# Performance work log

Hardware: AMD Instinct MI355X
Metric: run time of the kernel (lower is better)

## Reference

```python
import jax, jax.numpy as jnp
import numpy as np
import math

N = 50000      # nodes per type
E = 800000     # edges per relation
IN = 256
OUT = 256
H = 8
DK = OUT // H  # 32
SQRT_DK = math.sqrt(DK)


def setup_inputs() -> dict:
    key = jax.random.key(0)
    ks = jax.random.split(key, 24)
    s = 0.02
    inp = {
        'h_A': jax.random.normal(ks[0], (N, IN), jnp.float32),
        'h_B': jax.random.normal(ks[1], (N, IN), jnp.float32),
        'src0': jax.random.randint(ks[2], (E,), 0, N, jnp.int32),
        'dst0': jax.random.randint(ks[3], (E,), 0, N, jnp.int32),
        'src1': jax.random.randint(ks[4], (E,), 0, N, jnp.int32),
        'dst1': jax.random.randint(ks[5], (E,), 0, N, jnp.int32),
        'src2': jax.random.randint(ks[6], (E,), 0, N, jnp.int32),
        'dst2': jax.random.randint(ks[7], (E,), 0, N, jnp.int32),
        # per-node-type linears (2 types): y = x @ W + b
        'Wk': jax.random.normal(ks[8], (2, IN, OUT), jnp.float32) * s,
        'bk': jnp.zeros((2, OUT), jnp.float32),
        'Wq': jax.random.normal(ks[9], (2, IN, OUT), jnp.float32) * s,
        'bq': jnp.zeros((2, OUT), jnp.float32),
        'Wv': jax.random.normal(ks[10], (2, IN, OUT), jnp.float32) * s,
        'bv': jnp.zeros((2, OUT), jnp.float32),
        'Wa': jax.random.normal(ks[11], (2, OUT, OUT), jnp.float32) * s,
        'ba': jnp.zeros((2, OUT), jnp.float32),
        # per-relation params (3 relations)
        'rel_att': jax.random.normal(ks[12], (3, H, DK, DK), jnp.float32) * (1.0 / math.sqrt(DK)),
        'rel_msg': jax.random.normal(ks[13], (3, H, DK, DK), jnp.float32) * (1.0 / math.sqrt(DK)),
        'rel_pri': jnp.ones((3, H), jnp.float32),
        'skip': jnp.ones((2,), jnp.float32),
    }
    return inp


def _relation_flow(k_src, v_src, q_dst, A_r, M_r, pri_r, src, dst):
    # k_src/v_src/q_dst: [N,H,DK] ; A_r,M_r: [H,DK,DK] ; pri_r: [H]
    k = jnp.einsum('bij,ijk->bik', k_src, A_r)
    v = jnp.einsum('bij,ijk->bik', v_src, M_r)
    # edge-wise dot: sum_d q[dst] * k[src] per head -> [E,H]
    score = jnp.einsum('ehd,ehd->eh', q_dst[dst], k[src]) * pri_r / SQRT_DK
    # edge softmax normalized by dst
    mx = jax.ops.segment_max(score, dst, num_segments=N)
    ex = jnp.exp(score - mx[dst])
    den = jax.ops.segment_sum(ex, dst, num_segments=N)
    attn = ex / den[dst]                       # [E,H]
    msg = v[src] * attn[:, :, None]            # [E,H,DK]
    return jax.ops.segment_sum(msg, dst, num_segments=N)  # [N,H,DK]


def reference(h_A, h_B, src0, dst0, src1, dst1, src2, dst2,
              Wk, bk, Wq, bq, Wv, bv, Wa, ba,
              rel_att, rel_msg, rel_pri, skip):
    h = [h_A, h_B]
    hd = lambda x: x.reshape(-1, H, DK)
    k = [hd(h[t] @ Wk[t] + bk[t]) for t in range(2)]
    q = [hd(h[t] @ Wq[t] + bq[t]) for t in range(2)]
    v = [hd(h[t] @ Wv[t] + bv[t]) for t in range(2)]

    # relations: r0: A->B, r1: B->A, r2: A->B
    t0 = _relation_flow(k[0], v[0], q[1], rel_att[0], rel_msg[0], rel_pri[0], src0, dst0)
    t1 = _relation_flow(k[1], v[1], q[0], rel_att[1], rel_msg[1], rel_pri[1], src1, dst1)
    t2 = _relation_flow(k[0], v[0], q[1], rel_att[2], rel_msg[2], rel_pri[2], src2, dst2)

    # cross_reducer='mean' over relations delivering to each dst type
    t_A = t1.reshape(N, OUT)
    t_B = ((t0 + t2) * 0.5).reshape(N, OUT)

    def out_for(tn, nid):
        alpha = jax.nn.sigmoid(skip[nid])
        trans = tn @ Wa[nid] + ba[nid]   # dropout is identity at eval
        return trans * alpha + h[nid] * (1.0 - alpha)

    new_h_A = out_for(t_A, 0)
    new_h_B = out_for(t_B, 1)
    return jnp.stack([new_h_A, new_h_B])  # [2, N, OUT]
```

## Files before the change

kernel.cpp:

```cpp
#include <hip/hip_runtime.h>
#include <math.h>

#define NN 50000
#define EE 800000
#define CC 256
#define NS (NN * CC)
#define NBK 782
#define BCAP 2048
#define P1T 2048
#define NT1 391
#define TOBF_BLKS 12500
#define PREP_BLKS 2568

typedef __attribute__((ext_vector_type(4))) float f32x4;
typedef __attribute__((ext_vector_type(8))) short bf16x8;
typedef __attribute__((ext_vector_type(4))) unsigned int u32x4;
typedef __attribute__((ext_vector_type(2))) unsigned int u32x2;

__device__ __forceinline__ float bf2f(unsigned int u) {
    union { unsigned int i; float f; } c; c.i = u << 16; return c.f;
}
__device__ __forceinline__ unsigned short f2bf(float f) {
    union { float f; unsigned int i; } c; c.f = f;
    unsigned int u = c.i;
    u += 0x7fffu + ((u >> 16) & 1u);
    return (unsigned short)(u >> 16);
}

#if __has_builtin(__builtin_amdgcn_cvt_f32_fp8) && __has_builtin(__builtin_amdgcn_cvt_pk_fp8_f32)
#define HW_FP8 1
#else
#define HW_FP8 0
#endif

__device__ __forceinline__ unsigned char sw_f2fp8(float f) {
    float a = fabsf(f);
    unsigned s = (f < 0.f) ? 0x80u : 0u;
    if (a >= 448.f) return (unsigned char)(s | 0x7Eu);
    if (a < 0.015625f) {
        int q = (int)(a * 512.f + 0.5f);
        return (unsigned char)(s | (unsigned)q);
    }
    int e = (int)floorf(log2f(a));
    float m = ldexpf(a, -e);
    int q = (int)(m * 8.f + 0.5f);
    if (q == 16) { q = 8; e += 1; }
    if (e > 8) return (unsigned char)(s | 0x7Eu);
    return (unsigned char)(s | ((unsigned)(e + 7) << 3) | (unsigned)(q - 8));
}
__device__ __forceinline__ float sw_fp82f(unsigned b) {
    unsigned s = (b & 0x80u) << 24;
    unsigned exp = (b >> 3) & 0xFu, man = b & 7u;
    float val = (exp == 0) ? ldexpf((float)man, -9)
                           : ldexpf((float)(8u | man), (int)exp - 10);
    unsigned r = __builtin_bit_cast(unsigned, val) | s;
    return __builtin_bit_cast(float, r);
}
__device__ __forceinline__ unsigned char f2fp8(float f) {
#if HW_FP8
    return (unsigned char)(__builtin_amdgcn_cvt_pk_fp8_f32(f, 0.f, 0, false) & 0xff);
#else
    return sw_f2fp8(f);
#endif
}
__device__ __forceinline__ float fp8sel(unsigned int w, int sel) {
#if HW_FP8
    switch (sel) {
        case 0: return __builtin_amdgcn_cvt_f32_fp8((int)w, 0);
        case 1: return __builtin_amdgcn_cvt_f32_fp8((int)w, 1);
        case 2: return __builtin_amdgcn_cvt_f32_fp8((int)w, 2);
        default: return __builtin_amdgcn_cvt_f32_fp8((int)w, 3);
    }
#else
    return sw_fp82f((w >> (sel * 8)) & 0xffu);
#endif
}

__global__ void setup_kernel(const float* __restrict__ hA, const float* __restrict__ hB,
                             unsigned short* __restrict__ h_bf,
                             const float* __restrict__ Wk, const float* __restrict__ bk,
                             const float* __restrict__ Wq, const float* __restrict__ bq,
                             const float* __restrict__ Wv, const float* __restrict__ bv,
                             const float* __restrict__ Wa,
                             const float* __restrict__ rel_att, const float* __restrict__ rel_msg,
                             unsigned short* __restrict__ WT, float* __restrict__ ball,
                             const int* __restrict__ d0, const int* __restrict__ d1,
                             const int* __restrict__ d2, int* __restrict__ bcnt)
{
    int b = blockIdx.x;
    const int ts[3] = {0, 1, 0};
    if (b < TOBF_BLKS) {
        int id = b * 256 + threadIdx.x;
        size_t base = (size_t)id * 8;
        const float* src = (base < (size_t)NS) ? (hA + base) : (hB + (base - NS));
        f32x4 a = *(const f32x4*)src;
        f32x4 bb2 = *(const f32x4*)(src + 4);
        u32x4 o;
        o[0] = (unsigned)f2bf(a[0]) | ((unsigned)f2bf(a[1]) << 16);
        o[1] = (unsigned)f2bf(a[2]) | ((unsigned)f2bf(a[3]) << 16);
        o[2] = (unsigned)f2bf(bb2[0]) | ((unsigned)f2bf(bb2[1]) << 16);
        o[3] = (unsigned)f2bf(bb2[2]) | ((unsigned)f2bf(bb2[3]) << 16);
        *(u32x4*)(h_bf + base) = o;
        return;
    }
    if (b >= TOBF_BLKS + PREP_BLKS) {
        int bb = b - (TOBF_BLKS + PREP_BLKS);
        int r = bb / NT1, tile = bb - r * NT1;
        const int* dp = r == 0 ? d0 : (r == 1 ? d1 : d2);
        __shared__ int hist[NBK];
        for (int i = threadIdx.x; i < NBK; i += 256) hist[i] = 0;
        __syncthreads();
        int base = tile * P1T;
        int lim = base + P1T; if (lim > EE) lim = EE;
        for (int i = base + threadIdx.x; i < lim; i += 256)
            atomicAdd(&hist[dp[i] >> 6], 1);
        __syncthreads();
        for (int i = threadIdx.x; i < NBK; i += 256)
            if (hist[i]) atomicAdd(&bcnt[r * NBK + i], hist[i]);
        return;
    }
    int id = (b - TOBF_BLKS) * 256 + threadIdx.x;
    if (id < 2 * 65536) {
        int t = id >> 16, rem = id & 65535;
        int n = rem >> 8, k = rem & 255;
        WT[t * 65536 + n * 256 + k] = f2bf(Wq[t * 65536 + k * 256 + n]);
    } else if (id < 5 * 65536) {
        int id2 = id - 2 * 65536;
        int r = id2 >> 16, rem = id2 & 65535;
        int n = rem >> 8, k = rem & 255;
        int h = n >> 5, j = n & 31;
        const float* wkb = Wk + ts[r] * 65536 + k * 256 + h * 32;
        const float* ab  = rel_att + r * 8192 + h * 1024 + j;
        float s = 0.f;
        #pragma unroll 8
        for (int d = 0; d < 32; ++d) s += wkb[d] * ab[d * 32];
        WT[(2 + r) * 65536 + n * 256 + k] = f2bf(s);
    } else if (id < 8 * 65536) {
        int id2 = id - 5 * 65536;
        int r = id2 >> 16, rem = id2 & 65535;
        int n = rem >> 8, k = rem & 255;
        int h = n >> 5, j = n & 31;
        const float* wvb = Wv + ts[r] * 65536 + k * 256 + h * 32;
        const float* mb  = rel_msg + r * 8192 + h * 1024 + j;
        float s = 0.f;
        #pragma unroll 8
        for (int d = 0; d < 32; ++d) s += wvb[d] * mb[d * 32];
        WT[(5 + r) * 65536 + n * 256 + k] = f2bf(s);
    } else if (id < 10 * 65536) {
        int id2 = id - 8 * 65536;
        int t = id2 >> 16, rem = id2 & 65535;
        int n = rem >> 8, k = rem & 255;
        WT[(8 + t) * 65536 + n * 256 + k] = f2bf(Wa[t * 65536 + k * 256 + n]);
    } else if (id < 10 * 65536 + 2048) {
        int id2 = id - 10 * 65536;
        int z = id2 >> 8, c = id2 & 255;
        float v;
        if (z < 2) {
            v = bq[z * 256 + c];
        } else if (z < 5) {
            int r = z - 2, h = c >> 5, j = c & 31;
            const float* bkb = bk + ts[r] * 256 + h * 32;
            const float* ab  = rel_att + r * 8192 + h * 1024 + j;
            v = 0.f;
            for (int d = 0; d < 32; ++d) v += bkb[d] * ab[d * 32];
        } else {
            int r = z - 5, h = c >> 5, j = c & 31;
            const float* bvb = bv + ts[r] * 256 + h * 32;
            const float* mb  = rel_msg + r * 8192 + h * 1024 + j;
            v = 0.f;
            for (int d = 0; d < 32; ++d) v += bvb[d] * mb[d * 32];
        }
        ball[z * 256 + c] = v;
    }
}

__global__ __launch_bounds__(1024) void bscan_kernel(const int* __restrict__ bcnt,
                                                     int* __restrict__ bbase,
                                                     int* __restrict__ bcur)
{
    int r = blockIdx.x;
    int t = threadIdx.x, lane = t & 63, w = t >> 6;
    __shared__ int wsum[16];
    int x = (t < NBK) ? bcnt[r * NBK + t] : 0;
    int v = x;
    #pragma unroll
    for (int ofs = 1; ofs < 64; ofs <<= 1) {
        int y = __shfl_up(v, ofs);
        if (lane >= ofs) v += y;
    }
    if (lane == 63) wsum[w] = v;
    __syncthreads();
    if (t < 16) {
        int wv = wsum[t];
        #pragma unroll
        for (int ofs = 1; ofs < 16; ofs <<= 1) {
            int y = __shfl_up(wv, ofs);
            if (t >= ofs) wv += y;
        }
        wsum[t] = wv;
    }
    __syncthreads();
    int excl = (w > 0 ? wsum[w - 1] : 0) + v - x;
    if (t < NBK) { bbase[r * (NBK + 1) + t] = excl; bcur[r * NBK + t] = excl; }
    if (t == NBK - 1) bbase[r * (NBK + 1) + NBK] = excl + x;
}

__global__ __launch_bounds__(256) void p1_kernel(const int* __restrict__ s0, const int* __restrict__ s1,
                                                 const int* __restrict__ s2,
                                                 const int* __restrict__ d0, const int* __restrict__ d1,
                                                 const int* __restrict__ d2,
                                                 int* __restrict__ bcur, unsigned int* __restrict__ srcS)
{
    int bb = blockIdx.x;
    int r = bb / NT1, tile = bb - r * NT1;
    const int* sp = r == 0 ? s0 : (r == 1 ? s1 : s2);
    const int* dp = r == 0 ? d0 : (r == 1 ? d1 : d2);
    __shared__ int hist[NBK];
    __shared__ int lbase[NBK];
    for (int i = threadIdx.x; i < NBK; i += 256) hist[i] = 0;
    __syncthreads();
    int base = tile * P1T;
    int lim = base + P1T; if (lim > EE) lim = EE;
    for (int i = base + threadIdx.x; i < lim; i += 256)
        atomicAdd(&hist[dp[i] >> 6], 1);
    __syncthreads();
    for (int i = threadIdx.x; i < NBK; i += 256)
        lbase[i] = hist[i] ? atomicAdd(&bcur[r * NBK + i], hist[i]) : 0;
    __syncthreads();
    unsigned int* out = srcS + (size_t)r * EE;
    for (int i = base + threadIdx.x; i < lim; i += 256) {
        int dv = dp[i];
        int bk = dv >> 6;
        int pos = atomicAdd(&lbase[bk], 1);
        out[pos] = ((unsigned)sp[i] << 6) | (unsigned)(dv & 63);
    }
}

__global__ __launch_bounds__(256) void p2_kernel(const int* __restrict__ bbase,
                                                 unsigned int* __restrict__ srcS,
                                                 int* __restrict__ offs)
{
    int r = blockIdx.x / NBK, bk = blockIdx.x - r * NBK;
    int base = bbase[r * (NBK + 1) + bk];
    int n = bbase[r * (NBK + 1) + bk + 1] - base;
    unsigned int* seg = srcS + (size_t)r * EE + base;
    __shared__ unsigned int vals[BCAP];
    __shared__ unsigned int sorted[BCAP];
    __shared__ int hist[64], hcur[64];
    int t = threadIdx.x;
    if (t < 64) hist[t] = 0;
    __syncthreads();
    for (int i = t; i < n; i += 256) {
        unsigned int v = seg[i];
        vals[i] = v;
        atomicAdd(&hist[v & 63], 1);
    }
    __syncthreads();
    if (t < 64) {
        int x = hist[t], v = x;
        #pragma unroll
        for (int ofs = 1; ofs < 64; ofs <<= 1) {
            int y = __shfl_up(v, ofs);
            if (t >= ofs) v += y;
        }
        int excl = v - x;
        hcur[t] = excl;
        int d = bk * 64 + t;
        if (d < NN) offs[r * (NN + 1) + d] = base + excl;
    }
    if (bk == NBK - 1 && t == 64) offs[r * (NN + 1) + NN] = EE;
    __syncthreads();
    for (int i = t; i < n; i += 256) {
        unsigned int v = vals[i];
        int pos = atomicAdd(&hcur[v & 63], 1);
        sorted[pos] = v >> 6;
    }
    __syncthreads();
    for (int i = t; i < n; i += 256) seg[i] = sorted[i];
}

__device__ __forceinline__ void gemm_body(const unsigned short* __restrict__ A,
                                          const unsigned short* __restrict__ W,
                                          const float* __restrict__ bias,
                                          unsigned short* __restrict__ Obf,
                                          unsigned char* __restrict__ Of8,
                                          int mBase, int nBase)
{
    __shared__ __align__(16) unsigned short As[128 * 64];
    __shared__ __align__(16) unsigned short Bs[128 * 64];

    int tid = threadIdx.x;
    int lane = tid & 63, wid = tid >> 6;
    int warpM = wid >> 1, warpN = wid & 1;

    f32x4 acc[4][4];
    #pragma unroll
    for (int i = 0; i < 4; ++i)
        #pragma unroll
        for (int j = 0; j < 4; ++j) acc[i][j] = (f32x4){0.f, 0.f, 0.f, 0.f};

    for (int kt = 0; kt < 4; ++kt) {
        int k0 = kt * 64;
        __syncthreads();
        #pragma unroll
        for (int i = 0; i < 4; ++i) {
            int c = tid + i * 256;
            int row = c >> 3, cc = c & 7;
            int gr = mBase + row; if (gr > NN - 1) gr = NN - 1;
            u32x4 av = *(const u32x4*)(A + (size_t)gr * CC + k0 + cc * 8);
            int sb = row * 128 + ((cc * 16) ^ ((row & 7) << 4));
            *(u32x4*)((char*)As + sb) = av;
            u32x4 bv = *(const u32x4*)(W + (nBase + row) * 256 + k0 + cc * 8);
            *(u32x4*)((char*)Bs + sb) = bv;
        }
        __syncthreads();
        #pragma unroll
        for (int kk = 0; kk < 2; ++kk) {
            bf16x8 af[4], bfr[4];
            int kb = kk * 64 + (lane >> 4) * 16;
            #pragma unroll
            for (int mi = 0; mi < 4; ++mi) {
                int row = warpM * 64 + mi * 16 + (lane & 15);
                int sb = row * 128 + (kb ^ ((row & 7) << 4));
                af[mi] = *(const bf16x8*)((const char*)As + sb);
            }
            #pragma unroll
            for (int ni = 0; ni < 4; ++ni) {
                int row = warpN * 64 + ni * 16 + (lane & 15);
                int sb = row * 128 + (kb ^ ((row & 7) << 4));
                bfr[ni] = *(const bf16x8*)((const char*)Bs + sb);
            }
            #pragma unroll
            for (int mi = 0; mi < 4; ++mi)
                #pragma unroll
                for (int ni = 0; ni < 4; ++ni)
                    acc[mi][ni] = __builtin_amdgcn_mfma_f32_16x16x32_bf16(af[mi], bfr[ni], acc[mi][ni], 0, 0, 0);
        }
    }

    #pragma unroll
    for (int mi = 0; mi < 4; ++mi) {
        #pragma unroll
        for (int ni = 0; ni < 4; ++ni) {
            int col = nBase + warpN * 64 + ni * 16 + (lane & 15);
            int row0 = mBase + warpM * 64 + mi * 16 + (lane >> 4) * 4;
            float b = bias[col];
            #pragma unroll
            for (int j = 0; j < 4; ++j) {
                int row = row0 + j;
                if (row < NN) {
                    float val = acc[mi][ni][j] + b;
                    if (Of8) Of8[(size_t)row * 512 + col] = f2fp8(val);
                    else     Obf[(size_t)row * 256 + col] = f2bf(val);
                }
            }
        }
    }
}

__global__ __launch_bounds__(256, 2)
void gemm8_kernel(const unsigned short* __restrict__ h_bf,
                  const unsigned short* __restrict__ WT, const float* __restrict__ ball,
                  unsigned short* __restrict__ Qb, unsigned char* __restrict__ KV0,
                  unsigned char* __restrict__ KV1, unsigned char* __restrict__ KV2)
{
    int bid = blockIdx.x;
    int mtile = bid >> 4;
    int rem = bid & 15;
    int z = rem >> 1;
    int ntile = rem & 1;
    const unsigned short* A = (z == 1 || z == 3 || z == 6) ? (h_bf + (size_t)NS) : h_bf;
    unsigned short* Obf = nullptr;
    unsigned char* Of8 = nullptr;
    switch (z) {
        case 0: Obf = Qb;               break;
        case 1: Obf = Qb + (size_t)NS;  break;
        case 2: Of8 = KV0;              break;
        case 3: Of8 = KV1;              break;
        case 4: Of8 = KV2;              break;
        case 5: Of8 = KV0 + 256;        break;
        case 6: Of8 = KV1 + 256;        break;
        default: Of8 = KV2 + 256;       break;
    }
    gemm_body(A, WT + z * 65536, ball + z * 256, Obf, Of8,
              mtile * 128, ntile * 128);
}

__global__ __launch_bounds__(256, 2)
void out_gemm_kernel(const unsigned short* __restrict__ A0, const unsigned short* __restrict__ A1,
                     const unsigned short* __restrict__ W0, const unsigned short* __restrict__ W1,
                     const float* __restrict__ b0, const float* __restrict__ b1,
                     float* __restrict__ OutF,
                     const float* __restrict__ hA, const float* __restrict__ hB,
                     const float* __restrict__ skip)
{
    int z = blockIdx.z;
    const unsigned short* A = z ? A1 : A0;
    const unsigned short* W = z ? W1 : W0;
    const float* bias = z ? b1 : b0;
    int mBase = blockIdx.x * 128;
    int nBase = blockIdx.y * 128;

    __shared__ __align__(16) unsigned short As[128 * 64];
    __shared__ __align__(16) unsigned short Bs[128 * 64];

    int tid = threadIdx.x;
    int lane = tid & 63, wid = tid >> 6;
    int warpM = wid >> 1, warpN = wid & 1;

    f32x4 acc[4][4];
    #pragma unroll
    for (int i = 0; i < 4; ++i)
        #pragma unroll
        for (int j = 0; j < 4; ++j) acc[i][j] = (f32x4){0.f, 0.f, 0.f, 0.f};

    for (int kt = 0; kt < 4; ++kt) {
        int k0 = kt * 64;
        __syncthreads();
        #pragma unroll
        for (int i = 0; i < 4; ++i) {
            int c = tid + i * 256;
            int row = c >> 3, cc = c & 7;
            int gr = mBase + row; if (gr > NN - 1) gr = NN - 1;
            u32x4 av = *(const u32x4*)(A + (size_t)gr * CC + k0 + cc * 8);
            int sb = row * 128 + ((cc * 16) ^ ((row & 7) << 4));
            *(u32x4*)((char*)As + sb) = av;
            u32x4 bv = *(const u32x4*)(W + (nBase + row) * 256 + k0 + cc * 8);
            *(u32x4*)((char*)Bs + sb) = bv;
        }
        __syncthreads();
        #pragma unroll
        for (int kk = 0; kk < 2; ++kk) {
            bf16x8 af[4], bfr[4];
            int kb = kk * 64 + (lane >> 4) * 16;
            #pragma unroll
            for (int mi = 0; mi < 4; ++mi) {
                int row = warpM * 64 + mi * 16 + (lane & 15);
                int sb = row * 128 + (kb ^ ((row & 7) << 4));
                af[mi] = *(const bf16x8*)((const char*)As + sb);
            }
            #pragma unroll
            for (int ni = 0; ni < 4; ++ni) {
                int row = warpN * 64 + ni * 16 + (lane & 15);
                int sb = row * 128 + (kb ^ ((row & 7) << 4));
                bfr[ni] = *(const bf16x8*)((const char*)Bs + sb);
            }
            #pragma unroll
            for (int mi = 0; mi < 4; ++mi)
                #pragma unroll
                for (int ni = 0; ni < 4; ++ni)
                    acc[mi][ni] = __builtin_amdgcn_mfma_f32_16x16x32_bf16(af[mi], bfr[ni], acc[mi][ni], 0, 0, 0);
        }
    }

    float alpha = 1.f / (1.f + __expf(-skip[z]));
    const float* hres = z ? hB : hA;

    #pragma unroll
    for (int mi = 0; mi < 4; ++mi) {
        #pragma unroll
        for (int ni = 0; ni < 4; ++ni) {
            int col = nBase + warpN * 64 + ni * 16 + (lane & 15);
            int row0 = mBase + warpM * 64 + mi * 16 + (lane >> 4) * 4;
            float b = bias[col];
            #pragma unroll
            for (int j = 0; j < 4; ++j) {
                int row = row0 + j;
                if (row < NN) {
                    float val = acc[mi][ni][j] + b;
                    float hv = hres[(size_t)row * CC + col];
                    OutF[(size_t)z * NS + (size_t)row * CC + col] = val * alpha + hv * (1.f - alpha);
                }
            }
        }
    }
}

__device__ __forceinline__ void agg_pass(const unsigned char* __restrict__ KV,
                                         const int* __restrict__ srcS,
                                         int beg, int end, int lane,
                                         float q0, float q1, float q2, float q3, float ps,
                                         float& o0, float& o1, float& o2, float& o3)
{
    float l = 0.f;
    float a0 = 0.f, a1 = 0.f, a2 = 0.f, a3 = 0.f;
    int n = end - beg;
    if (n > 0) {
        int p0 = beg + lane;
        int idx = srcS[p0 < end ? p0 : end - 1];
        int s = __shfl(idx, 0);
        unsigned int kw = *(const unsigned int*)(KV + (size_t)s * 512 + lane * 4);
        unsigned int vw = *(const unsigned int*)(KV + (size_t)s * 512 + 256 + lane * 4);
        for (int j = 0; j < n; ++j) {
            unsigned int kc = kw, vc = vw;
            int jn = j + 1;
            if (jn < n) {
                if ((jn & 63) == 0) {
                    int p = beg + jn + lane;
                    idx = srcS[p < end ? p : end - 1];
                }
                int sn = __shfl(idx, jn & 63);
                kw = *(const unsigned int*)(KV + (size_t)sn * 512 + lane * 4);
                vw = *(const unsigned int*)(KV + (size_t)sn * 512 + 256 + lane * 4);
            }
            float d = q0 * fp8sel(kc, 0) + q1 * fp8sel(kc, 1)
                    + q2 * fp8sel(kc, 2) + q3 * fp8sel(kc, 3);
            d += __shfl_xor(d, 1);
            d += __shfl_xor(d, 2);
            d += __shfl_xor(d, 4);
            float pw = __expf(d * ps);
            l += pw;
            a0 += pw * fp8sel(vc, 0);
            a1 += pw * fp8sel(vc, 1);
            a2 += pw * fp8sel(vc, 2);
            a3 += pw * fp8sel(vc, 3);
        }
    }
    float inv = (l > 0.f) ? 1.f / l : 0.f;
    o0 = a0 * inv; o1 = a1 * inv; o2 = a2 * inv; o3 = a3 * inv;
}

__global__ __launch_bounds__(256)
void agg_all_kernel(const unsigned short* __restrict__ Q0, const unsigned short* __restrict__ Q1,
                    const unsigned char* __restrict__ KV0, const unsigned char* __restrict__ KV1,
                    const unsigned char* __restrict__ KV2,
                    const int* __restrict__ offs, const int* __restrict__ srcS,
                    const float* __restrict__ rel_pri,
                    unsigned short* __restrict__ TbA, unsigned short* __restrict__ TbB)
{
    int w = (blockIdx.x * 256 + threadIdx.x) >> 6;
    int lane = threadIdx.x & 63;
    int h = lane >> 3;
    const float rs = 0.17677669529663687f;

    if (w < NN) {
        int d = w;
        u32x2 qv = *(const u32x2*)(Q1 + (size_t)d * CC + lane * 4);
        float q0 = bf2f(qv[0] & 0xffffu), q1 = bf2f(qv[0] >> 16);
        float q2 = bf2f(qv[1] & 0xffffu), q3 = bf2f(qv[1] >> 16);
        float x0, x1, x2, x3, y0, y1, y2, y3;
        agg_pass(KV0, (const int*)srcS, offs[d], offs[d + 1], lane,
                 q0, q1, q2, q3, rel_pri[h] * rs, x0, x1, x2, x3);
        const int* off2 = offs + 2 * (NN + 1);
        agg_pass(KV2, (const int*)srcS + 2 * EE, off2[d], off2[d + 1], lane,
                 q0, q1, q2, q3, rel_pri[16 + h] * rs, y0, y1, y2, y3);
        unsigned short* out = TbB + (size_t)d * CC + lane * 4;
        u32x2 o;
        o[0] = (unsigned)f2bf((x0 + y0) * 0.5f) | ((unsigned)f2bf((x1 + y1) * 0.5f) << 16);
        o[1] = (unsigned)f2bf((x2 + y2) * 0.5f) | ((unsigned)f2bf((x3 + y3) * 0.5f) << 16);
        *(u32x2*)out = o;
    } else if (w < 2 * NN) {
        int d = w - NN;
        u32x2 qv = *(const u32x2*)(Q0 + (size_t)d * CC + lane * 4);
        float q0 = bf2f(qv[0] & 0xffffu), q1 = bf2f(qv[0] >> 16);
        float q2 = bf2f(qv[1] & 0xffffu), q3 = bf2f(qv[1] >> 16);
        float x0, x1, x2, x3;
        const int* off1 = offs + (NN + 1);
        agg_pass(KV1, (const int*)srcS + EE, off1[d], off1[d + 1], lane,
                 q0, q1, q2, q3, rel_pri[8 + h] * rs, x0, x1, x2, x3);
        unsigned short* out = TbA + (size_t)d * CC + lane * 4;
        u32x2 o;
        o[0] = (unsigned)f2bf(x0) | ((unsigned)f2bf(x1) << 16);
        o[1] = (unsigned)f2bf(x2) | ((unsigned)f2bf(x3) << 16);
        *(u32x2*)out = o;
    }
}

extern "C" void kernel_launch(void* const* d_in, const int* in_sizes, int n_in,
                              void* d_out, int out_size, void* d_ws, size_t ws_size,
                              hipStream_t stream)
{
    const float* hA = (const float*)d_in[0];
    const float* hB = (const float*)d_in[1];
    const int* src0 = (const int*)d_in[2];
    const int* dst0 = (const int*)d_in[3];
    const int* src1 = (const int*)d_in[4];
    const int* dst1 = (const int*)d_in[5];
    const int* src2 = (const int*)d_in[6];
    const int* dst2 = (const int*)d_in[7];
    const float* Wk = (const float*)d_in[8];
    const float* bk = (const float*)d_in[9];
    const float* Wq = (const float*)d_in[10];
    const float* bq = (const float*)d_in[11];
    const float* Wv = (const float*)d_in[12];
    const float* bv = (const float*)d_in[13];
    const float* Wa = (const float*)d_in[14];
    const float* ba = (const float*)d_in[15];
    const float* rel_att = (const float*)d_in[16];
    const float* rel_msg = (const float*)d_in[17];
    const float* rel_pri = (const float*)d_in[18];
    const float* skip = (const float*)d_in[19];

    char* w = (char*)d_ws;
    auto alloc = [&](size_t bytes) {
        char* p = w;
        w += (bytes + 255) & ~(size_t)255;
        return p;
    };
    unsigned short* WT  = (unsigned short*)alloc((size_t)10 * 65536 * 2);
    float* ball         = (float*)alloc((size_t)8 * 256 * 4);
    unsigned short* Qb  = (unsigned short*)alloc((size_t)2 * NS * 2);
    unsigned char* KV0  = (unsigned char*)alloc((size_t)NN * 512);
    unsigned short* Tb  = (unsigned short*)alloc((size_t)2 * NS * 2);
    int* offs           = (int*)alloc((size_t)3 * (NN + 1) * 4);
    int* srcS           = (int*)alloc((size_t)3 * EE * 4);
    int* bcnt           = (int*)alloc((size_t)3 * NBK * 4);
    int* bbase          = (int*)alloc((size_t)3 * (NBK + 1) * 4);
    int* bcur           = (int*)alloc((size_t)3 * NBK * 4);

    unsigned char* dob = (unsigned char*)d_out;
    unsigned char* KV1 = dob;
    unsigned char* KV2 = dob + (size_t)NN * 512;
    unsigned short* h_bf = (unsigned short*)(dob + (size_t)2 * NN * 512);

    (void)hipMemsetAsync(bcnt, 0, (size_t)3 * NBK * 4, stream);

    setup_kernel<<<TOBF_BLKS + PREP_BLKS + 3 * NT1, 256, 0, stream>>>(
        hA, hB, h_bf, Wk, bk, Wq, bq, Wv, bv, Wa,
        rel_att, rel_msg, WT, ball, dst0, dst1, dst2, bcnt);
    bscan_kernel<<<3, 1024, 0, stream>>>(bcnt, bbase, bcur);
    p1_kernel<<<3 * NT1, 256, 0, stream>>>(src0, src1, src2, dst0, dst1, dst2,
                                           bcur, (unsigned int*)srcS);
    p2_kernel<<<3 * NBK, 256, 0, stream>>>(bbase, (unsigned int*)srcS, offs);

    gemm8_kernel<<<391 * 16, 256, 0, stream>>>(h_bf, WT, ball, Qb, KV0, KV1, KV2);

    agg_all_kernel<<<25000, 256, 0, stream>>>(Qb, Qb + NS, KV0, KV1, KV2,
                                              offs, srcS, rel_pri, Tb, Tb + NS);

    out_gemm_kernel<<<dim3(391, 2, 2), 256, 0, stream>>>(
        Tb, Tb + NS, WT + 8 * 65536, WT + 9 * 65536, ba, ba + 256,
        (float*)d_out, hA, hB, skip);
}
```

Measured before the change: 526.8 us.

## Split relation aggregation into per-relation warps and average in output GEMM

```diff
diff --git a/kernel.cpp b/kernel.cpp
--- a/kernel.cpp
+++ b/kernel.cpp
@@ -13,6 +13,7 @@
 #define PREP_BLKS 2568
 
 typedef __attribute__((ext_vector_type(4))) float f32x4;
+typedef __attribute__((ext_vector_type(2))) float f32x2;
 typedef __attribute__((ext_vector_type(8))) short bf16x8;
 typedef __attribute__((ext_vector_type(4))) unsigned int u32x4;
 typedef __attribute__((ext_vector_type(2))) unsigned int u32x2;
@@ -31,6 +32,11 @@
 #define HW_FP8 1
 #else
 #define HW_FP8 0
+#endif
+#if __has_builtin(__builtin_amdgcn_cvt_pk_f32_fp8)
+#define HW_FP8PK 1
+#else
+#define HW_FP8PK 0
 #endif
 
 __device__ __forceinline__ unsigned char sw_f2fp8(float f) {
@@ -63,16 +69,15 @@
     return sw_f2fp8(f);
 #endif
 }
-__device__ __forceinline__ float fp8sel(unsigned int w, int sel) {
-#if HW_FP8
-    switch (sel) {
-        case 0: return __builtin_amdgcn_cvt_f32_fp8((int)w, 0);
-        case 1: return __builtin_amdgcn_cvt_f32_fp8((int)w, 1);
-        case 2: return __builtin_amdgcn_cvt_f32_fp8((int)w, 2);
-        default: return __builtin_amdgcn_cvt_f32_fp8((int)w, 3);
-    }
+template<bool HI>
+__device__ __forceinline__ f32x2 fp8pair(unsigned int w) {
+#if HW_FP8PK
+    return __builtin_amdgcn_cvt_pk_f32_fp8((int)w, HI);
 #else
-    return sw_fp82f((w >> (sel * 8)) & 0xffu);
+    f32x2 r;
+    r[0] = sw_fp82f((w >> (HI ? 16 : 0)) & 0xffu);
+    r[1] = sw_fp82f((w >> (HI ? 24 : 8)) & 0xffu);
+    return r;
 #endif
 }
 
@@ -388,6 +393,7 @@
 
 __global__ __launch_bounds__(256, 2)
 void out_gemm_kernel(const unsigned short* __restrict__ A0, const unsigned short* __restrict__ A1,
+                     const unsigned short* __restrict__ A1b,
                      const unsigned short* __restrict__ W0, const unsigned short* __restrict__ W1,
                      const float* __restrict__ b0, const float* __restrict__ b1,
                      float* __restrict__ OutF,
@@ -422,7 +428,17 @@
             int c = tid + i * 256;
             int row = c >> 3, cc = c & 7;
             int gr = mBase + row; if (gr > NN - 1) gr = NN - 1;
-            u32x4 av = *(const u32x4*)(A + (size_t)gr * CC + k0 + cc * 8);
+            size_t aofs = (size_t)gr * CC + k0 + cc * 8;
+            u32x4 av = *(const u32x4*)(A + aofs);
+            if (z) {
+                u32x4 av2 = *(const u32x4*)(A1b + aofs);
+                #pragma unroll
+                for (int q = 0; q < 4; ++q) {
+                    float lo = (bf2f(av[q] & 0xffffu) + bf2f(av2[q] & 0xffffu)) * 0.5f;
+                    float hi = (bf2f(av[q] >> 16) + bf2f(av2[q] >> 16)) * 0.5f;
+                    av[q] = (unsigned)f2bf(lo) | ((unsigned)f2bf(hi) << 16);
+                }
+            }
             int sb = row * 128 + ((cc * 16) ^ ((row & 7) << 4));
             *(u32x4*)((char*)As + sb) = av;
             u32x4 bv = *(const u32x4*)(W + (nBase + row) * 256 + k0 + cc * 8);
@@ -479,7 +495,7 @@
 __device__ __forceinline__ void agg_pass(const unsigned char* __restrict__ KV,
                                          const int* __restrict__ srcS,
                                          int beg, int end, int lane,
-                                         float q0, float q1, float q2, float q3, float ps,
+                                         float q0, float q1, float q2, float q3, float ps2,
                                          float& o0, float& o1, float& o2, float& o3)
 {
     float l = 0.f;
@@ -503,17 +519,18 @@
                 kw = *(const unsigned int*)(KV + (size_t)sn * 512 + lane * 4);
                 vw = *(const unsigned int*)(KV + (size_t)sn * 512 + 256 + lane * 4);
             }
-            float d = q0 * fp8sel(kc, 0) + q1 * fp8sel(kc, 1)
-                    + q2 * fp8sel(kc, 2) + q3 * fp8sel(kc, 3);
+            f32x2 k01 = fp8pair<false>(kc), k23 = fp8pair<true>(kc);
+            float d = fmaf(q0, k01[0], fmaf(q1, k01[1], fmaf(q2, k23[0], q3 * k23[1])));
             d += __shfl_xor(d, 1);
             d += __shfl_xor(d, 2);
             d += __shfl_xor(d, 4);
-            float pw = __expf(d * ps);
+            float pw = exp2f(d * ps2);
             l += pw;
-            a0 += pw * fp8sel(vc, 0);
-            a1 += pw * fp8sel(vc, 1);
-            a2 += pw * fp8sel(vc, 2);
-            a3 += pw * fp8sel(vc, 3);
+            f32x2 v01 = fp8pair<false>(vc), v23 = fp8pair<true>(vc);
+            a0 = fmaf(pw, v01[0], a0);
+            a1 = fmaf(pw, v01[1], a1);
+            a2 = fmaf(pw, v23[0], a2);
+            a3 = fmaf(pw, v23[1], a3);
         }
     }
     float inv = (l > 0.f) ? 1.f / l : 0.f;
@@ -526,44 +543,33 @@
                     const unsigned char* __restrict__ KV2,
                     const int* __restrict__ offs, const int* __restrict__ srcS,
                     const float* __restrict__ rel_pri,
-                    unsigned short* __restrict__ TbA, unsigned short* __restrict__ TbB)
+                    unsigned short* __restrict__ TbA, unsigned short* __restrict__ TbB,
+                    unsigned short* __restrict__ T2b)
 {
     int w = (blockIdx.x * 256 + threadIdx.x) >> 6;
+    if (w >= 3 * NN) return;
     int lane = threadIdx.x & 63;
     int h = lane >> 3;
-    const float rs = 0.17677669529663687f;
-
-    if (w < NN) {
-        int d = w;
-        u32x2 qv = *(const u32x2*)(Q1 + (size_t)d * CC + lane * 4);
-        float q0 = bf2f(qv[0] & 0xffffu), q1 = bf2f(qv[0] >> 16);
-        float q2 = bf2f(qv[1] & 0xffffu), q3 = bf2f(qv[1] >> 16);
-        float x0, x1, x2, x3, y0, y1, y2, y3;
-        agg_pass(KV0, (const int*)srcS, offs[d], offs[d + 1], lane,
-                 q0, q1, q2, q3, rel_pri[h] * rs, x0, x1, x2, x3);
-        const int* off2 = offs + 2 * (NN + 1);
-        agg_pass(KV2, (const int*)srcS + 2 * EE, off2[d], off2[d + 1], lane,
-                 q0, q1, q2, q3, rel_pri[16 + h] * rs, y0, y1, y2, y3);
-        unsigned short* out = TbB + (size_t)d * CC + lane * 4;
-        u32x2 o;
-        o[0] = (unsigned)f2bf((x0 + y0) * 0.5f) | ((unsigned)f2bf((x1 + y1) * 0.5f) << 16);
-        o[1] = (unsigned)f2bf((x2 + y2) * 0.5f) | ((unsigned)f2bf((x3 + y3) * 0.5f) << 16);
-        *(u32x2*)out = o;
-    } else if (w < 2 * NN) {
-        int d = w - NN;
-        u32x2 qv = *(const u32x2*)(Q0 + (size_t)d * CC + lane * 4);
-        float q0 = bf2f(qv[0] & 0xffffu), q1 = bf2f(qv[0] >> 16);
-        float q2 = bf2f(qv[1] & 0xffffu), q3 = bf2f(qv[1] >> 16);
-        float x0, x1, x2, x3;
-        const int* off1 = offs + (NN + 1);
-        agg_pass(KV1, (const int*)srcS + EE, off1[d], off1[d + 1], lane,
-                 q0, q1, q2, q3, rel_pri[8 + h] * rs, x0, x1, x2, x3);
-        unsigned short* out = TbA + (size_t)d * CC + lane * 4;
-        u32x2 o;
-        o[0] = (unsigned)f2bf(x0) | ((unsigned)f2bf(x1) << 16);
-        o[1] = (unsigned)f2bf(x2) | ((unsigned)f2bf(x3) << 16);
-        *(u32x2*)out = o;
-    }
+    const float rs2 = 0.17677669529663687f * 1.4426950408889634f;
+
+    int r = (w < NN) ? 0 : (w < 2 * NN ? 1 : 2);
+    int d = w - r * NN;
+    const unsigned short* Q = (r == 1) ? Q0 : Q1;
+    const unsigned char* KV = (r == 0) ? KV0 : (r == 1 ? KV1 : KV2);
+    unsigned short* T = (r == 0) ? TbB : (r == 1 ? TbA : T2b);
+
+    u32x2 qv = *(const u32x2*)(Q + (size_t)d * CC + lane * 4);
+    float q0 = bf2f(qv[0] & 0xffffu), q1 = bf2f(qv[0] >> 16);
+    float q2 = bf2f(qv[1] & 0xffffu), q3 = bf2f(qv[1] >> 16);
+    const int* off = offs + r * (NN + 1);
+    float x0, x1, x2, x3;
+    agg_pass(KV, (const int*)srcS + (size_t)r * EE, off[d], off[d + 1], lane,
+             q0, q1, q2, q3, rel_pri[r * 8 + h] * rs2, x0, x1, x2, x3);
+    unsigned short* out = T + (size_t)d * CC + lane * 4;
+    u32x2 o;
+    o[0] = (unsigned)f2bf(x0) | ((unsigned)f2bf(x1) << 16);
+    o[1] = (unsigned)f2bf(x2) | ((unsigned)f2bf(x3) << 16);
+    *(u32x2*)out = o;
 }
 
 extern "C" void kernel_launch(void* const* d_in, const int* in_sizes, int n_in,
@@ -602,6 +608,7 @@
     unsigned short* Qb  = (unsigned short*)alloc((size_t)2 * NS * 2);
     unsigned char* KV0  = (unsigned char*)alloc((size_t)NN * 512);
     unsigned short* Tb  = (unsigned short*)alloc((size_t)2 * NS * 2);
+    unsigned short* T2b = (unsigned short*)alloc((size_t)NS * 2);
     int* offs           = (int*)alloc((size_t)3 * (NN + 1) * 4);
     int* srcS           = (int*)alloc((size_t)3 * EE * 4);
     int* bcnt           = (int*)alloc((size_t)3 * NBK * 4);
@@ -625,10 +632,11 @@
 
     gemm8_kernel<<<391 * 16, 256, 0, stream>>>(h_bf, WT, ball, Qb, KV0, KV1, KV2);
 
-    agg_all_kernel<<<25000, 256, 0, stream>>>(Qb, Qb + NS, KV0, KV1, KV2,
-                                              offs, srcS, rel_pri, Tb, Tb + NS);
+    agg_all_kernel<<<37500, 256, 0, stream>>>(Qb, Qb + NS, KV0, KV1, KV2,
+                                              offs, srcS, rel_pri,
+                                              Tb, Tb + NS, T2b);
 
     out_gemm_kernel<<<dim3(391, 2, 2), 256, 0, stream>>>(
-        Tb, Tb + NS, WT + 8 * 65536, WT + 9 * 65536, ba, ba + 256,
+        Tb, Tb + NS, T2b, WT + 8 * 65536, WT + 9 * 65536, ba, ba + 256,
         (float*)d_out, hA, hB, skip);
 }
```

Measured after the change: 564.0 us. 7.1% more time.
